# Kernel tuning notes

Measured on AMD Instinct MI355X. Metric: run time of the kernel, lower is better.

The kernel has to match this reference:

```python
import jax, jax.numpy as jnp
import numpy as np

N_NODES = 20000
N_EDGES = 640000
K_RADIAL = 16
N_TYPES = 8


def setup_inputs() -> dict:
    key = jax.random.key(0)
    k1, k2, k3, k4 = jax.random.split(key, 4)
    # distances in (0.1, 12] Angstrom
    distances = jax.random.uniform(k1, (N_EDGES, 1), dtype=jnp.float32, minval=0.1, maxval=12.0)
    # radial params: [cutoff, mean, scaling] per kernel (ACNN defaults)
    cutoffs = jnp.full((K_RADIAL,), 12.0, dtype=jnp.float32)
    means = jnp.arange(K_RADIAL, dtype=jnp.float32) * (12.0 / K_RADIAL)
    scaling = jnp.full((K_RADIAL,), 4.0, dtype=jnp.float32)
    radial_params = jnp.stack([cutoffs, means, scaling], axis=1)  # (K,3)
    features_to_use = jnp.array([1.0, 6.0, 7.0, 8.0, 9.0, 15.0, 16.0, 17.0], dtype=jnp.float32)
    # node features: atomic numbers in [0,18)
    feat = jax.random.randint(k2, (N_NODES, 1), 0, 18).astype(jnp.float32)
    src = jax.random.randint(k3, (N_EDGES,), 0, N_NODES, dtype=jnp.int32)
    dst = jax.random.randint(k4, (N_EDGES,), 0, N_NODES, dtype=jnp.int32)
    return {"feat": feat, "distances": distances, "radial_params": radial_params,
            "features_to_use": features_to_use, "src": src, "dst": dst}


def radial_pooling(distances, radial_params):
    # params broadcast as (K,1,1) against distances (E,1) -> (K,E,1)
    cutoffs = radial_params[:, 0].reshape(-1, 1, 1)
    means = radial_params[:, 1].reshape(-1, 1, 1)
    scaling = radial_params[:, 2].reshape(-1, 1, 1)
    rbf = jnp.exp(-scaling * (distances - means) ** 2)
    cos_vals = 0.5 * (jnp.cos(jnp.float32(np.pi) * distances / cutoffs) + 1.0)
    cutoff_vals = jnp.where(distances <= cutoffs, cos_vals, jnp.zeros_like(cos_vals))
    return rbf * cutoff_vals  # (K,E,1)


def reference(feat, distances, radial_params, features_to_use, src, dst):
    n_nodes = feat.shape[0]
    n_edges = distances.shape[0]
    # edge weights; faithful reshape (K,E,1) -> (E,K) as in the torch code
    he = radial_pooling(distances, radial_params).reshape(n_edges, -1)  # (E,K)
    # one-hot encode atomic numbers against features_to_use
    hv = (feat.reshape(-1, 1) == features_to_use[None, :]).astype(jnp.float32)
    hv = hv.reshape(n_nodes, -1)[:, :, None]  # (N,T,1)
    # gather src features, multiply by edge weights, scatter-sum to dst
    m = hv[src] * he[:, None, :]  # (E,T,K)
    hv_new = jax.ops.segment_sum(m, dst, num_segments=n_nodes)  # (N,T,K)
    return hv_new.reshape(n_nodes, -1)  # (N, T*K)
```

## Files before the change

kernel.cpp:

```cpp
#include <hip/hip_runtime.h>
#include <math.h>

#define N_NODES 20000
#define N_EDGES 640000
#define K_RADIAL 16
#define N_TYPES 8
#define E_PER_K (N_EDGES / K_RADIAL)
#define CAP 64
#define GCAP 48


__device__ __forceinline__ int type_of(float v, const float* __restrict__ f2u) {
    int t = -1;
#pragma unroll
    for (int j = 0; j < N_TYPES; ++j)
        if (v == f2u[j]) t = j;
    return t;
}

__global__ void __launch_bounds__(256) scatter_kernel(
    const float* __restrict__ feat, const float* __restrict__ f2u,
    const int* __restrict__ src, const int* __restrict__ dst,
    int* __restrict__ cnt, int* __restrict__ bucket) {
    int tid = blockIdx.x * blockDim.x + threadIdx.x;
    if (tid >= N_EDGES / 4) return;
    int4 s4 = ((const int4*)src)[tid];
    int4 d4 = ((const int4*)dst)[tid];
    int e0 = tid * 4;
    int sv[4] = {s4.x, s4.y, s4.z, s4.w};
    int dv[4] = {d4.x, d4.y, d4.z, d4.w};
#pragma unroll
    for (int c = 0; c < 4; ++c) {
        int t = type_of(feat[sv[c]], f2u);
        if (t < 0) continue;
        int e = e0 + c;
        int k = e / E_PER_K;
        int base = (e - k * E_PER_K) * 16;
        int d = dv[c];
        int pos = atomicAdd(&cnt[d], 1);
        if (pos < CAP)
            bucket[d * CAP + pos] = base | (k << 20) | (t << 24);
    }
}

__global__ void __launch_bounds__(256) gather_kernel(
    const int* __restrict__ cnt, const int* __restrict__ bucket,
    const float* __restrict__ dist, const float* __restrict__ rp,
    float* __restrict__ out) {
    __shared__ float4 prm[K_RADIAL];
    if (threadIdx.x < K_RADIAL) {
        int lt = threadIdx.x;
        float c = rp[3 * lt + 0];
        float m = rp[3 * lt + 1];
        float s = rp[3 * lt + 2];
        prm[lt] = make_float4(c, m, s, __fdividef(3.14159265358979323846f, c));
    }
    __syncthreads();

    int node = blockIdx.x * 4 + (threadIdx.x >> 6);
    if (node >= N_NODES) return;
    int lane = threadIdx.x & 63;
    int kp = lane & 15;
    int sub = lane >> 4;

    int n = cnt[node];
    if (n < 0) n = 0;
    if (n > GCAP) n = GCAP;
    const int* bp = bucket + node * CAP;

    float acc[N_TYPES];
#pragma unroll
    for (int t = 0; t < N_TYPES; ++t) acc[t] = 0.0f;

    for (int c0 = 0; c0 < GCAP; c0 += 16) {
        if (c0 >= n) break;
        int p[4];
        float dd[4];
#pragma unroll
        for (int i = 0; i < 4; ++i) {
            int j = c0 + sub + 4 * i;
            p[i] = (j < n) ? bp[j] : -1;
        }
#pragma unroll
        for (int i = 0; i < 4; ++i)
            dd[i] = (p[i] >= 0) ? dist[(p[i] & 0xFFFFF) + kp] : 1e30f;
#pragma unroll
        for (int i = 0; i < 4; ++i) {
            int k = (p[i] >> 20) & 15;
            int te = (p[i] >> 24) & 7;
            float4 q = prm[k];
            float d = dd[i];
            float dm = d - q.y;
            float rbf = __expf(-q.z * dm * dm);
            float cv = 0.5f * (__cosf(q.w * d) + 1.0f);
            float w = (d <= q.x) ? rbf * cv : 0.0f;
#pragma unroll
            for (int t = 0; t < N_TYPES; ++t)
                acc[t] += (t == te) ? w : 0.0f;
        }
    }

#pragma unroll
    for (int t = 0; t < N_TYPES; ++t) {
        acc[t] += __shfl_xor(acc[t], 16, 64);
        acc[t] += __shfl_xor(acc[t], 32, 64);
    }

    float* op = out + (size_t)node * (N_TYPES * K_RADIAL);
    op[lane] = acc[sub];
    op[64 + lane] = acc[4 + sub];
}

extern "C" void kernel_launch(void* const* d_in, const int* in_sizes, int n_in,
                              void* d_out, int out_size, void* d_ws, size_t ws_size,
                              hipStream_t stream) {
    const float* feat = (const float*)d_in[0];
    const float* dist = (const float*)d_in[1];
    const float* rp   = (const float*)d_in[2];
    const float* f2u  = (const float*)d_in[3];
    const int*   src  = (const int*)d_in[4];
    const int*   dst  = (const int*)d_in[5];
    float* out = (float*)d_out;

    int* cnt    = (int*)d_ws;
    int* bucket = cnt + 20480;

    hipMemsetAsync(cnt, 0, N_NODES * sizeof(int), stream);
    scatter_kernel<<<(N_EDGES / 4 + 255) / 256, 256, 0, stream>>>(feat, f2u, src, dst, cnt, bucket);
    gather_kernel<<<(N_NODES + 3) / 4, 256, 0, stream>>>(cnt, bucket, dist, rp, out);
}
```

Measured before the change: 102.6 us.

## Fuse memset, scatter and gather into one cooperative kernel with grid syncs

Replaces the memset plus two kernel launches with a single cooperative persistent kernel. It zeroes the counters, buckets edges, then gathers per node, with grid-wide barriers between phases. The gather runs as a grid-stride loop over nodes per wave. This removes launch gaps and inter-kernel idle time, but adds grid-sync cost and caps occupancy at a fixed grid size. The old path is kept as a fallback if the cooperative launch fails.

After: 288.9 us. 2.82x slower.

```diff
diff --git a/kernel.cpp b/kernel.cpp
--- a/kernel.cpp
+++ b/kernel.cpp
@@ -1,5 +1,8 @@
 #include <hip/hip_runtime.h>
+#include <hip/hip_cooperative_groups.h>
 #include <math.h>
+
+namespace cg = cooperative_groups;
 
 #define N_NODES 20000
 #define N_EDGES 640000
@@ -9,6 +12,11 @@
 #define CAP 64
 #define GCAP 48
 
+#define NBLK 1024
+#define NTHR 256
+#define NTHREADS (NBLK * NTHR)
+#define NWAVES (NTHREADS / 64)
+
 
 __device__ __forceinline__ int type_of(float v, const float* __restrict__ f2u) {
     int t = -1;
@@ -17,6 +25,104 @@
         if (v == f2u[j]) t = j;
     return t;
 }
+
+__global__ void __launch_bounds__(NTHR, 4) fused_kernel(
+    const float* __restrict__ feat, const float* __restrict__ dist,
+    const float* __restrict__ rp, const float* __restrict__ f2u,
+    const int* __restrict__ src, const int* __restrict__ dst,
+    float* __restrict__ out, int* __restrict__ cnt, int* __restrict__ bucket)
+{
+    cg::grid_group grid = cg::this_grid();
+    const int tid = blockIdx.x * NTHR + threadIdx.x;
+
+    __shared__ float4 prm[K_RADIAL];
+    if (threadIdx.x < K_RADIAL) {
+        int lt = threadIdx.x;
+        float c = rp[3 * lt + 0];
+        float m = rp[3 * lt + 1];
+        float s = rp[3 * lt + 2];
+        prm[lt] = make_float4(c, m, s, __fdividef(3.14159265358979323846f, c));
+    }
+
+    if (tid < N_NODES) cnt[tid] = 0;
+    grid.sync();
+
+    if (tid < N_EDGES / 4) {
+        int4 s4 = ((const int4*)src)[tid];
+        int4 d4 = ((const int4*)dst)[tid];
+        int e0 = tid * 4;
+        int sv[4] = {s4.x, s4.y, s4.z, s4.w};
+        int dv[4] = {d4.x, d4.y, d4.z, d4.w};
+#pragma unroll
+        for (int c = 0; c < 4; ++c) {
+            int t = type_of(feat[sv[c]], f2u);
+            if (t < 0) continue;
+            int e = e0 + c;
+            int k = e / E_PER_K;
+            int base = (e - k * E_PER_K) * 16;
+            int d = dv[c];
+            int pos = atomicAdd(&cnt[d], 1);
+            if (pos < CAP)
+                bucket[d * CAP + pos] = base | (k << 20) | (t << 24);
+        }
+    }
+    grid.sync();
+
+    const int lane = threadIdx.x & 63;
+    const int kp = lane & 15;
+    const int sub = lane >> 4;
+    const int wave = tid >> 6;
+
+    for (int node = wave; node < N_NODES; node += NWAVES) {
+        int n = cnt[node];
+        if (n < 0) n = 0;
+        if (n > GCAP) n = GCAP;
+        const int* bp = bucket + node * CAP;
+
+        float acc[N_TYPES];
+#pragma unroll
+        for (int t = 0; t < N_TYPES; ++t) acc[t] = 0.0f;
+
+        for (int c0 = 0; c0 < GCAP; c0 += 16) {
+            if (c0 >= n) break;
+            int p[4];
+            float dd[4];
+#pragma unroll
+            for (int i = 0; i < 4; ++i) {
+                int j = c0 + sub + 4 * i;
+                p[i] = (j < n) ? bp[j] : -1;
+            }
+#pragma unroll
+            for (int i = 0; i < 4; ++i)
+                dd[i] = (p[i] >= 0) ? dist[(p[i] & 0xFFFFF) + kp] : 1e30f;
+#pragma unroll
+            for (int i = 0; i < 4; ++i) {
+                int k = (p[i] >> 20) & 15;
+                int te = (p[i] >> 24) & 7;
+                float4 q = prm[k];
+                float d = dd[i];
+                float dm = d - q.y;
+                float rbf = __expf(-q.z * dm * dm);
+                float cv = 0.5f * (__cosf(q.w * d) + 1.0f);
+                float w = (d <= q.x) ? rbf * cv : 0.0f;
+#pragma unroll
+                for (int t = 0; t < N_TYPES; ++t)
+                    acc[t] += (t == te) ? w : 0.0f;
+            }
+        }
+
+#pragma unroll
+        for (int t = 0; t < N_TYPES; ++t) {
+            acc[t] += __shfl_xor(acc[t], 16, 64);
+            acc[t] += __shfl_xor(acc[t], 32, 64);
+        }
+
+        float* op = out + (size_t)node * (N_TYPES * K_RADIAL);
+        op[lane] = acc[sub];
+        op[64 + lane] = acc[4 + sub];
+    }
+}
+
 
 __global__ void __launch_bounds__(256) scatter_kernel(
     const float* __restrict__ feat, const float* __restrict__ f2u,
@@ -125,7 +231,14 @@
     int* cnt    = (int*)d_ws;
     int* bucket = cnt + 20480;
 
-    hipMemsetAsync(cnt, 0, N_NODES * sizeof(int), stream);
-    scatter_kernel<<<(N_EDGES / 4 + 255) / 256, 256, 0, stream>>>(feat, f2u, src, dst, cnt, bucket);
-    gather_kernel<<<(N_NODES + 3) / 4, 256, 0, stream>>>(cnt, bucket, dist, rp, out);
-}
+    void* args[] = {(void*)&feat, (void*)&dist, (void*)&rp, (void*)&f2u,
+                    (void*)&src, (void*)&dst, (void*)&out, (void*)&cnt, (void*)&bucket};
+    hipError_t err = hipLaunchCooperativeKernel((const void*)fused_kernel,
+                                                dim3(NBLK), dim3(NTHR),
+                                                args, 0, stream);
+    if (err != hipSuccess) {
+        hipMemsetAsync(cnt, 0, N_NODES * sizeof(int), stream);
+        scatter_kernel<<<(N_EDGES / 4 + 255) / 256, 256, 0, stream>>>(feat, f2u, src, dst, cnt, bucket);
+        gather_kernel<<<(N_NODES + 3) / 4, 256, 0, stream>>>(cnt, bucket, dist, rp, out);
+    }
+}
```
